# Kernel optimization log

Measured on AMD Instinct MI355X. Metric: run time of the kernel, lower is better.

The kernel has to match this reference:

```python
import jax, jax.numpy as jnp
import numpy as np

H = 16       # num_attention_heads
HKV = 4      # num_key_value_heads
G = H // HKV # num_kv_groups
D = 128      # head_dim
ROT = 64     # rotary dim = head_dim * rope_partial_rotary_factor (0.5)
BLK = 64     # sparse_block_size
LOCAL = 8    # sparse_local_num_blocks
GLOB = 1     # sparse_global_num_blocks
SCALE = 1.0 / float(np.sqrt(D))
NEG = -1000000000.0


def _rotate_half(x):
    x1, x2 = x[..., : x.shape[-1] // 2], x[..., x.shape[-1] // 2 :]
    return jnp.concatenate((-x2, x1), axis=-1)


def _sparse_tables(n_blocks):
    """Static numpy tables mirroring _get_sparse_tables + causal masking.
    Returns idx (n,S) int32 gather table and mask (n, BLK, S, BLK) bool (True = masked)."""
    S = LOCAL + GLOB
    idx = np.zeros((n_blocks, S), np.int32)
    valid = np.zeros((n_blocks, S), bool)
    for i in range(n_blocks):
        sel = [g for g in range(GLOB) if g < n_blocks]
        sel += list(range(max(0, i - (LOCAL - 1)), i + 1))
        li = list(dict.fromkeys(sel))  # dedupe, keep order
        idx[i, : len(li)] = li
        valid[i, : len(li)] = True
    ii = np.arange(n_blocks)[:, None]
    dead = (~valid) | (idx > ii)          # invalid slot or future block
    selfb = idx == ii                     # diagonal block -> intra-causal
    jq = np.arange(BLK)[:, None]
    jk = np.arange(BLK)[None, :]
    intra = jk > jq                       # (q, k) strictly-upper masked
    mask = dead[:, None, :, None] | (selfb[:, None, :, None] & intra[None, :, None, :])
    return idx, mask                      # (n,S), (n,BLK,S,BLK)


def setup_inputs() -> dict:
    key = jax.random.key(0)
    ks = jax.random.split(key, 6)
    B_, T, HID = 2, 4096, 2048
    hidden_states = jax.random.normal(ks[0], (B_, T, HID), dtype=jnp.float32)
    # real RoPE tables for the rotary sub-dim
    inv_freq = 1.0 / (10000.0 ** (np.arange(0, ROT, 2, dtype=np.float32) / ROT))
    freqs = np.arange(T, dtype=np.float32)[:, None] * inv_freq[None, :]
    emb = np.concatenate([freqs, freqs], axis=-1)  # (T, ROT)
    cos = jnp.broadcast_to(jnp.asarray(np.cos(emb)), (B_, T, ROT))
    sin = jnp.broadcast_to(jnp.asarray(np.sin(emb)), (B_, T, ROT))
    Wq = jax.random.normal(ks[1], (H * D, HID), dtype=jnp.float32) * 0.02
    Wk = jax.random.normal(ks[2], (HKV * D, HID), dtype=jnp.float32) * 0.02
    Wv = jax.random.normal(ks[3], (HKV * D, HID), dtype=jnp.float32) * 0.02
    Wo = jax.random.normal(ks[4], (HID, H * D), dtype=jnp.float32) * 0.02
    return {"hidden_states": hidden_states, "cos": cos, "sin": sin,
            "Wq": Wq, "Wk": Wk, "Wv": Wv, "Wo": Wo}


def reference(hidden_states, cos, sin, Wq, Wk, Wv, Wo):
    B_, T, _ = hidden_states.shape
    q = (hidden_states @ Wq.T).reshape(B_, T, H, D).transpose(0, 2, 1, 3)    # (b,H,T,D)
    k = (hidden_states @ Wk.T).reshape(B_, T, HKV, D).transpose(0, 2, 1, 3)  # (b,HKV,T,D)
    v = (hidden_states @ Wv.T).reshape(B_, T, HKV, D).transpose(0, 2, 1, 3)
    # partial RoPE on first ROT dims
    c = cos[:, None, :, :]
    s = sin[:, None, :, :]
    def rope(x):
        xr, xp = x[..., :ROT], x[..., ROT:]
        xr = xr * c + _rotate_half(xr) * s
        return jnp.concatenate([xr, xp], axis=-1)
    q, k = rope(q), rope(k)
    # block-sparse local+global attention (prefill, T multiple of BLK)
    n = T // BLK
    idx_np, mask_np = _sparse_tables(n)
    idx = jnp.asarray(idx_np)
    mask = jnp.asarray(mask_np)  # (n, BLKq, S, BLKk)
    qb = q.reshape(B_, HKV, G, n, BLK, D)
    kb = k.reshape(B_, HKV, n, BLK, D)
    vb = v.reshape(B_, HKV, n, BLK, D)
    ksel = kb[:, :, idx]  # (b,HKV,n,S,BLK,D)
    vsel = vb[:, :, idx]
    scores = jnp.einsum('bhgnqd,bhnskd->bhgnqsk',
                        qb.astype(jnp.float32), ksel.astype(jnp.float32)) * SCALE
    scores = jnp.where(mask[None, None, None], NEG, scores)
    sh = scores.shape
    probs = jax.nn.softmax(scores.reshape(*sh[:5], -1), axis=-1).reshape(sh)
    out = jnp.einsum('bhgnqsk,bhnskd->bhgnqd', probs, vsel.astype(jnp.float32))
    out = out.astype(hidden_states.dtype).reshape(B_, H, T, D)
    out = out.transpose(0, 2, 1, 3).reshape(B_, T, H * D)
    return out @ Wo.T
```

## Files before the change

### kernel.cpp

```cpp
#include <hip/hip_runtime.h>
#include <hip/hip_bf16.h>

#define Hq   16
#define HKV  4
#define Dh   128
#define ROT  64
#define BLKQ 64
#define NBLK 64
#define Tlen 4096
#define Bsz  2
#define HID  2048
#define QKVC 3072
#define SCALE_C 0.08838834764831845f

typedef __attribute__((ext_vector_type(8))) short bf16x8;
typedef __attribute__((ext_vector_type(4))) float f32x4;

#define MFMA16(a, b, c) __builtin_amdgcn_mfma_f32_16x16x32_bf16((a), (b), (c), 0, 0, 0)

__device__ __forceinline__ void async_copy16(__hip_bfloat16* lds, const __hip_bfloat16* g) {
    __builtin_amdgcn_global_load_lds(
        (const __attribute__((address_space(1))) void*)g,
        (__attribute__((address_space(3))) void*)lds,
        16, 0, 0);
}

__global__ __launch_bounds__(256) void cvt_kernel(
    const float* __restrict__ s0, const float* __restrict__ s1,
    const float* __restrict__ s2, const float* __restrict__ s3,
    const float* __restrict__ s4,
    __hip_bfloat16* __restrict__ base,
    int n0, int n1, int n2, int n3, int n4)
{
    const float* src;
    size_t off, n;
    switch (blockIdx.y) {
        case 0:  src = s0; off = 0;                          n = n0; break;
        case 1:  src = s1; off = (size_t)n0;                 n = n1; break;
        case 2:  src = s2; off = (size_t)n0 + n1;            n = n2; break;
        case 3:  src = s3; off = (size_t)n0 + n1 + n2;       n = n3; break;
        default: src = s4; off = (size_t)n0 + n1 + n2 + n3;  n = n4; break;
    }
    __hip_bfloat16* dst = base + off;
    const size_t stride = (size_t)gridDim.x * 2048;
    for (size_t i = ((size_t)blockIdx.x * 256 + threadIdx.x) * 8; i < n; i += stride) {
        const float4 a = *(const float4*)(src + i);
        const float4 b = *(const float4*)(src + i + 4);
        union { bf16x8 v; __hip_bfloat16 e[8]; } u;
        u.e[0] = __float2bfloat16(a.x); u.e[1] = __float2bfloat16(a.y);
        u.e[2] = __float2bfloat16(a.z); u.e[3] = __float2bfloat16(a.w);
        u.e[4] = __float2bfloat16(b.x); u.e[5] = __float2bfloat16(b.y);
        u.e[6] = __float2bfloat16(b.z); u.e[7] = __float2bfloat16(b.w);
        *(bf16x8*)(dst + i) = u.v;
    }
}

template <bool ROPE_, bool F32OUT>
__global__ __launch_bounds__(512) void gemm256(
    const __hip_bfloat16* __restrict__ A,
    const __hip_bfloat16* __restrict__ B0,
    const __hip_bfloat16* __restrict__ B1,
    const __hip_bfloat16* __restrict__ B2,
    int n1c, int n2c,
    void* __restrict__ C,
    int M, int N, int K,
    const float* __restrict__ cosb,
    const float* __restrict__ sinb)
{
    __shared__ __align__(16) __hip_bfloat16 As[2][256 * 64];
    __shared__ __align__(16) __hip_bfloat16 Bs[2][256 * 64];

    const int gn  = N >> 8;
    const int nwg = (M >> 8) * gn;
    const int id  = blockIdx.x;
    const int swz = (id & 7) * (nwg >> 3) + (id >> 3);
    const int mt  = swz / gn;
    const int nt  = swz - mt * gn;
    const int m0  = mt << 8;
    const int n0  = nt << 8;

    const __hip_bfloat16* Bp;
    int nb;
    if (n0 < n1c)      { Bp = B0; nb = n0; }
    else if (n0 < n2c) { Bp = B1; nb = n0 - n1c; }
    else               { Bp = B2; nb = n0 - n2c; }

    const int tid  = threadIdx.x;
    const int lane = tid & 63;
    const int w    = tid >> 6;
    const int wm   = (w >> 2) << 7;
    const int wn   = (w & 3) << 6;
    const int m16  = lane & 15;
    const int q8   = lane >> 4;
    const int lr   = lane >> 3;
    const int lc   = lane & 7;
    const int cg   = lc ^ lr;
    const int NT   = K >> 6;

    f32x4 acc[8][4] = {};

    auto stageA = [&](int buf, int half, int kc) {
        #pragma unroll
        for (int is = 0; is < 2; ++is) {
            const int r8 = (half << 7) + (is << 6) + (w << 3);
            async_copy16(&As[buf][r8 << 6],
                         A + (size_t)(m0 + r8 + lr) * K + kc + (cg << 3));
        }
    };
    auto stageB = [&](int buf, int half, int kc) {
        #pragma unroll
        for (int is = 0; is < 2; ++is) {
            const int r8 = (half << 7) + (is << 6) + (w << 3);
            async_copy16(&Bs[buf][r8 << 6],
                         Bp + (size_t)(nb + r8 + lr) * K + kc + (cg << 3));
        }
    };

    stageA(0, 0, 0);  stageA(0, 1, 0);
    stageB(0, 0, 0);  stageB(0, 1, 0);
    stageA(1, 0, 64); stageA(1, 1, 64);
    asm volatile("s_waitcnt vmcnt(4)" ::: "memory");
    __builtin_amdgcn_s_barrier();

    for (int u = 0; u < NT; ++u) {
        const int P = u & 1;
        int tB = u + 1; if (tB >= NT) tB -= NT;
        int tA = u + 2; if (tA >= NT) tA -= NT;
        const int kB = tB << 6;
        const int kA = tA << 6;
        const __hip_bfloat16* Ap_ = As[P];
        const __hip_bfloat16* Bq_ = Bs[P];
        const int csl = m16 & 7;

        bf16x8 a0[8], b0[4], a1[8], b1[4];

        #pragma unroll
        for (int m = 0; m < 8; ++m) {
            const int row = wm + (m << 4) + m16;
            const int cs  = q8 ^ csl;
            a0[m] = *(const bf16x8*)&Ap_[(row << 6) + (cs << 3)];
        }
        #pragma unroll
        for (int n = 0; n < 4; ++n) {
            const int row = wn + (n << 4) + m16;
            const int cs  = q8 ^ csl;
            b0[n] = *(const bf16x8*)&Bq_[(row << 6) + (cs << 3)];
        }
        stageB(P ^ 1, 0, kB);
        __builtin_amdgcn_s_barrier();
        asm volatile("s_waitcnt lgkmcnt(0)" ::: "memory");
        __builtin_amdgcn_s_setprio(1);
        #pragma unroll
        for (int m = 0; m < 8; ++m) {
            acc[m][0] = MFMA16(a0[m], b0[0], acc[m][0]);
            acc[m][1] = MFMA16(a0[m], b0[1], acc[m][1]);
        }
        __builtin_amdgcn_s_setprio(0);
        __builtin_amdgcn_s_barrier();

        #pragma unroll
        for (int m = 0; m < 8; ++m) {
            const int row = wm + (m << 4) + m16;
            const int cs  = (4 + q8) ^ csl;
            a1[m] = *(const bf16x8*)&Ap_[(row << 6) + (cs << 3)];
        }
        stageB(P ^ 1, 1, kB);
        __builtin_amdgcn_s_barrier();
        __builtin_amdgcn_s_setprio(1);
        #pragma unroll
        for (int m = 0; m < 8; ++m) {
            acc[m][2] = MFMA16(a0[m], b0[2], acc[m][2]);
            acc[m][3] = MFMA16(a0[m], b0[3], acc[m][3]);
        }
        __builtin_amdgcn_s_setprio(0);
        __builtin_amdgcn_s_barrier();

        #pragma unroll
        for (int n = 0; n < 4; ++n) {
            const int row = wn + (n << 4) + m16;
            const int cs  = (4 + q8) ^ csl;
            b1[n] = *(const bf16x8*)&Bq_[(row << 6) + (cs << 3)];
        }
        __builtin_amdgcn_s_barrier();
        asm volatile("s_waitcnt lgkmcnt(0)" ::: "memory");
        __builtin_amdgcn_s_setprio(1);
        #pragma unroll
        for (int m = 0; m < 8; ++m) {
            acc[m][0] = MFMA16(a1[m], b1[0], acc[m][0]);
            acc[m][1] = MFMA16(a1[m], b1[1], acc[m][1]);
        }
        __builtin_amdgcn_s_setprio(0);
        __builtin_amdgcn_s_barrier();

        stageA(P, 0, kA);
        stageA(P, 1, kA);
        asm volatile("s_waitcnt vmcnt(4)" ::: "memory");
        __builtin_amdgcn_s_barrier();
        __builtin_amdgcn_s_setprio(1);
        #pragma unroll
        for (int m = 0; m < 8; ++m) {
            acc[m][2] = MFMA16(a1[m], b1[2], acc[m][2]);
            acc[m][3] = MFMA16(a1[m], b1[3], acc[m][3]);
        }
        __builtin_amdgcn_s_setprio(0);
        __builtin_amdgcn_s_barrier();
    }

    const int c0 = n0 + wn;
    if (ROPE_ && c0 < n2c && (c0 & 64) == 0) {
        #pragma unroll
        for (int i = 0; i < 8; ++i)
            #pragma unroll
            for (int r = 0; r < 4; ++r) {
                const int bt = m0 + wm + (i << 4) + (q8 << 2) + r;
                #pragma unroll
                for (int j = 0; j < 2; ++j) {
                    const int d = (j << 4) + m16;
                    const float c = cosb[(size_t)bt * ROT + d];
                    const float s = sinb[(size_t)bt * ROT + d];
                    const float x1 = acc[i][j][r];
                    const float x2 = acc[i][j + 2][r];
                    acc[i][j][r]     = x1 * c - x2 * s;
                    acc[i][j + 2][r] = x2 * c + x1 * s;
                }
            }
    }

    #pragma unroll
    for (int i = 0; i < 8; ++i)
        #pragma unroll
        for (int j = 0; j < 4; ++j)
            #pragma unroll
            for (int r = 0; r < 4; ++r) {
                const int row = m0 + wm + (i << 4) + (q8 << 2) + r;
                const int col = n0 + wn + (j << 4) + m16;
                if (F32OUT)
                    ((float*)C)[(size_t)row * N + col] = acc[i][j][r];
                else
                    ((__hip_bfloat16*)C)[(size_t)row * N + col] =
                        __float2bfloat16(acc[i][j][r]);
            }
}

__global__ __launch_bounds__(256) void attn_kernel(
    const __hip_bfloat16* __restrict__ qkv,
    __hip_bfloat16* __restrict__ outb)
{
    const int i   = blockIdx.x;
    const int h   = blockIdx.y;
    const int b   = blockIdx.z;
    const int kvh = h >> 2;
    const int tid  = threadIdx.x;
    const int lane = tid & 63;
    const int w    = tid >> 6;
    const int m16  = lane & 15;
    const int q8   = lane >> 4;

    __shared__ __align__(16) __hip_bfloat16 Ks[64 * 136];
    __shared__ __align__(16) __hip_bfloat16 VT[128 * 72];
    __shared__ __align__(16) __hip_bfloat16 Pb[4][16 * 72];

    bf16x8 qf[4];
    {
        const __hip_bfloat16* qp =
            qkv + (size_t)(b * Tlen + i * BLKQ + w * 16 + m16) * QKVC + h * Dh + q8 * 8;
        for (int ks = 0; ks < 4; ++ks) qf[ks] = *(const bf16x8*)(qp + ks * 32);
    }

    f32x4 o[8] = {};
    float mrow[4] = {-1e30f, -1e30f, -1e30f, -1e30f};
    float lrow[4] = {0.f, 0.f, 0.f, 0.f};

    const int nsel = (i + 1 < 9) ? (i + 1) : 9;
    for (int j = 0; j < nsel; ++j) {
        const int kb = (i <= 7) ? j : ((j == 0) ? 0 : (i - 8 + j));

        __syncthreads();
        {
            const __hip_bfloat16* kbase =
                qkv + (size_t)(b * Tlen + kb * BLKQ) * QKVC + HID + kvh * Dh;
            const __hip_bfloat16* vbase = kbase + 512;
            for (int c = tid; c < 1024; c += 256) {
                const int key = c >> 4;
                const int d0  = (c & 15) * 8;
                *(bf16x8*)&Ks[key * 136 + d0] =
                    *(const bf16x8*)(kbase + (size_t)key * QKVC + d0);
            }
            for (int c = tid; c < 1024; c += 256) {
                const int key = c & 63;
                const int d0  = (c >> 6) * 8;
                bf16x8 v8 = *(const bf16x8*)(vbase + (size_t)key * QKVC + d0);
                const __hip_bfloat16* ve = (const __hip_bfloat16*)&v8;
                for (int jj = 0; jj < 8; ++jj)
                    VT[(d0 + jj) * 72 + key] = ve[jj];
            }
        }
        __syncthreads();

        float sv[4][4];
        for (int nt = 0; nt < 4; ++nt) {
            f32x4 s = {0.f, 0.f, 0.f, 0.f};
            for (int ks = 0; ks < 4; ++ks) {
                bf16x8 kf = *(const bf16x8*)&Ks[(nt * 16 + m16) * 136 + ks * 32 + q8 * 8];
                s = MFMA16(qf[ks], kf, s);
            }
            for (int r = 0; r < 4; ++r) sv[nt][r] = s[r] * SCALE_C;
        }
        if (kb == i) {
            for (int nt = 0; nt < 4; ++nt) {
                const int key = nt * 16 + m16;
                for (int r = 0; r < 4; ++r) {
                    const int qr = w * 16 + q8 * 4 + r;
                    if (key > qr) sv[nt][r] = -1e9f;
                }
            }
        }

        float alpha[4];
        for (int r = 0; r < 4; ++r) {
            float mx = fmaxf(fmaxf(sv[0][r], sv[1][r]), fmaxf(sv[2][r], sv[3][r]));
            for (int off = 1; off < 16; off <<= 1) mx = fmaxf(mx, __shfl_xor(mx, off, 64));
            const float newm = fmaxf(mrow[r], mx);
            alpha[r] = __expf(mrow[r] - newm);
            mrow[r] = newm;
            float rs = 0.f;
            for (int nt = 0; nt < 4; ++nt) {
                const float p = __expf(sv[nt][r] - newm);
                sv[nt][r] = p;
                rs += p;
            }
            for (int off = 1; off < 16; off <<= 1) rs += __shfl_xor(rs, off, 64);
            lrow[r] = lrow[r] * alpha[r] + rs;
        }

        __hip_bfloat16* Pw = &Pb[w][0];
        for (int nt = 0; nt < 4; ++nt)
            for (int r = 0; r < 4; ++r)
                Pw[(q8 * 4 + r) * 72 + nt * 16 + m16] = __float2bfloat16(sv[nt][r]);

        for (int dt = 0; dt < 8; ++dt)
            for (int r = 0; r < 4; ++r)
                o[dt][r] *= alpha[r];

        __syncthreads();

        for (int kk = 0; kk < 2; ++kk) {
            bf16x8 pf = *(const bf16x8*)&Pw[m16 * 72 + kk * 32 + q8 * 8];
            for (int dt = 0; dt < 8; ++dt) {
                bf16x8 vf = *(const bf16x8*)&VT[(dt * 16 + m16) * 72 + kk * 32 + q8 * 8];
                o[dt] = MFMA16(pf, vf, o[dt]);
            }
        }
    }

    float rcp[4];
    for (int r = 0; r < 4; ++r) rcp[r] = 1.0f / lrow[r];
    __hip_bfloat16* op = outb + (size_t)(b * Tlen + i * BLKQ) * (Hq * Dh) + h * Dh;
    for (int dt = 0; dt < 8; ++dt)
        for (int r = 0; r < 4; ++r) {
            const float val = o[dt][r] * rcp[r];
            op[(size_t)(w * 16 + q8 * 4 + r) * (Hq * Dh) + dt * 16 + m16] =
                __float2bfloat16(val);
        }
}

extern "C" void kernel_launch(void* const* d_in, const int* in_sizes, int n_in,
                              void* d_out, int out_size, void* d_ws, size_t ws_size,
                              hipStream_t stream) {
    const float* hs   = (const float*)d_in[0];
    const float* cosb = (const float*)d_in[1];
    const float* sinb = (const float*)d_in[2];
    const float* Wq   = (const float*)d_in[3];
    const float* Wk   = (const float*)d_in[4];
    const float* Wv   = (const float*)d_in[5];
    const float* Wo   = (const float*)d_in[6];

    const int M = Bsz * Tlen;
    const int nHS = M * HID;
    const int nWq = Hq * Dh * HID;
    const int nWk = HKV * Dh * HID;
    const int nWv = nWk;
    const int nWo = HID * Hq * Dh;

    __hip_bfloat16* hsb  = (__hip_bfloat16*)d_ws;
    __hip_bfloat16* wqb  = hsb + nHS;
    __hip_bfloat16* wkb  = wqb + nWq;
    __hip_bfloat16* wvb  = wkb + nWk;
    __hip_bfloat16* wob  = wvb + nWv;
    __hip_bfloat16* qkv  = wob + nWo;
    __hip_bfloat16* attn = qkv + (size_t)M * QKVC;

    cvt_kernel<<<dim3(8192, 5), 256, 0, stream>>>(
        hs, Wq, Wk, Wv, Wo, hsb, nHS, nWq, nWk, nWv, nWo);
    gemm256<true, false><<<dim3((QKVC / 256) * (M / 256)), 512, 0, stream>>>(
        hsb, wqb, wkb, wvb, HID, HID + 512, qkv, M, QKVC, HID, cosb, sinb);
    attn_kernel<<<dim3(NBLK, Hq, Bsz), 256, 0, stream>>>(qkv, attn);
    gemm256<false, true><<<dim3((HID / 256) * (M / 256)), 512, 0, stream>>>(
        attn, wob, wob, wob, HID, HID, d_out, M, HID, HID, nullptr, nullptr);
}
```

Before: 479.8 us.

## Prefetch next K/V block into registers and relax attention sync

The attention loop now loads the next selected K/V block from global memory into registers while the current block is computed, then writes it to shared memory at the top of the next iteration. This hides global-load latency behind the MFMA work. The block-wide barrier before the P·V step is replaced by an LDS waitcnt, since each wave reads only its own P buffer. Wave priority hints are placed around the MFMA sections, and launch bounds now request 2 or 3 blocks per CU, which caps register use and risks spills alongside the extra prefetch registers.

```diff
diff --git a/kernel.cpp b/kernel.cpp
--- a/kernel.cpp
+++ b/kernel.cpp
@@ -56,7 +56,7 @@
 }
 
 template <bool ROPE_, bool F32OUT>
-__global__ __launch_bounds__(512) void gemm256(
+__global__ __launch_bounds__(512, 2) void gemm256(
     const __hip_bfloat16* __restrict__ A,
     const __hip_bfloat16* __restrict__ B0,
     const __hip_bfloat16* __restrict__ B1,
@@ -242,7 +242,7 @@
             }
 }
 
-__global__ __launch_bounds__(256) void attn_kernel(
+__global__ __launch_bounds__(256, 3) void attn_kernel(
     const __hip_bfloat16* __restrict__ qkv,
     __hip_bfloat16* __restrict__ outb)
 {
@@ -272,32 +272,56 @@
     float lrow[4] = {0.f, 0.f, 0.f, 0.f};
 
     const int nsel = (i + 1 < 9) ? (i + 1) : 9;
+    auto kb_of = [&](int j) { return (i <= 7) ? j : ((j == 0) ? 0 : (i - 8 + j)); };
+
+    bf16x8 kr[4], vr[4];
+    {
+        const __hip_bfloat16* kbase =
+            qkv + (size_t)(b * Tlen + kb_of(0) * BLKQ) * QKVC + HID + kvh * Dh;
+        const __hip_bfloat16* vbase = kbase + 512;
+        #pragma unroll
+        for (int t = 0; t < 4; ++t) {
+            const int c = tid + t * 256;
+            kr[t] = *(const bf16x8*)(kbase + (size_t)(c >> 4) * QKVC + (c & 15) * 8);
+            vr[t] = *(const bf16x8*)(vbase + (size_t)(c & 63) * QKVC + (c >> 6) * 8);
+        }
+    }
+
     for (int j = 0; j < nsel; ++j) {
-        const int kb = (i <= 7) ? j : ((j == 0) ? 0 : (i - 8 + j));
+        const int kb = kb_of(j);
 
         __syncthreads();
-        {
+        #pragma unroll
+        for (int t = 0; t < 4; ++t) {
+            const int c = tid + t * 256;
+            *(bf16x8*)&Ks[(c >> 4) * 136 + (c & 15) * 8] = kr[t];
+        }
+        #pragma unroll
+        for (int t = 0; t < 4; ++t) {
+            const int c = tid + t * 256;
+            const int key = c & 63;
+            const int d0  = (c >> 6) * 8;
+            const __hip_bfloat16* ve = (const __hip_bfloat16*)&vr[t];
+            #pragma unroll
+            for (int jj = 0; jj < 8; ++jj)
+                VT[(d0 + jj) * 72 + key] = ve[jj];
+        }
+        __syncthreads();
+
+        if (j + 1 < nsel) {
             const __hip_bfloat16* kbase =
-                qkv + (size_t)(b * Tlen + kb * BLKQ) * QKVC + HID + kvh * Dh;
+                qkv + (size_t)(b * Tlen + kb_of(j + 1) * BLKQ) * QKVC + HID + kvh * Dh;
             const __hip_bfloat16* vbase = kbase + 512;
-            for (int c = tid; c < 1024; c += 256) {
-                const int key = c >> 4;
-                const int d0  = (c & 15) * 8;
-                *(bf16x8*)&Ks[key * 136 + d0] =
-                    *(const bf16x8*)(kbase + (size_t)key * QKVC + d0);
-            }
-            for (int c = tid; c < 1024; c += 256) {
-                const int key = c & 63;
-                const int d0  = (c >> 6) * 8;
-                bf16x8 v8 = *(const bf16x8*)(vbase + (size_t)key * QKVC + d0);
-                const __hip_bfloat16* ve = (const __hip_bfloat16*)&v8;
-                for (int jj = 0; jj < 8; ++jj)
-                    VT[(d0 + jj) * 72 + key] = ve[jj];
-            }
-        }
-        __syncthreads();
+            #pragma unroll
+            for (int t = 0; t < 4; ++t) {
+                const int c = tid + t * 256;
+                kr[t] = *(const bf16x8*)(kbase + (size_t)(c >> 4) * QKVC + (c & 15) * 8);
+                vr[t] = *(const bf16x8*)(vbase + (size_t)(c & 63) * QKVC + (c >> 6) * 8);
+            }
+        }
 
         float sv[4][4];
+        __builtin_amdgcn_s_setprio(1);
         for (int nt = 0; nt < 4; ++nt) {
             f32x4 s = {0.f, 0.f, 0.f, 0.f};
             for (int ks = 0; ks < 4; ++ks) {
@@ -306,6 +330,7 @@
             }
             for (int r = 0; r < 4; ++r) sv[nt][r] = s[r] * SCALE_C;
         }
+        __builtin_amdgcn_s_setprio(0);
         if (kb == i) {
             for (int nt = 0; nt < 4; ++nt) {
                 const int key = nt * 16 + m16;
@@ -342,8 +367,10 @@
             for (int r = 0; r < 4; ++r)
                 o[dt][r] *= alpha[r];
 
-        __syncthreads();
-
+        asm volatile("s_waitcnt lgkmcnt(0)" ::: "memory");
+        __builtin_amdgcn_sched_barrier(0);
+
+        __builtin_amdgcn_s_setprio(1);
         for (int kk = 0; kk < 2; ++kk) {
             bf16x8 pf = *(const bf16x8*)&Pw[m16 * 72 + kk * 32 + q8 * 8];
             for (int dt = 0; dt < 8; ++dt) {
@@ -351,6 +378,7 @@
                 o[dt] = MFMA16(pf, vf, o[dt]);
             }
         }
+        __builtin_amdgcn_s_setprio(0);
     }
 
     float rcp[4];
```

New measurement: 450.8 us. 1.06x faster.
